# Kernel optimization log

Hardware: AMD Instinct MI355X
Metric: run time of the kernel (lower is better)

The kernel has to match this reference:

```python
import jax, jax.numpy as jnp
import numpy as np

B, T, D = 2, 2048, 1024
H = 16
DK = D // H


def setup_inputs() -> dict:
    key = jax.random.key(0)
    ks = jax.random.split(key, 5)
    s = 1.0 / np.sqrt(D)
    return {
        "x": jax.random.normal(ks[0], (B, T, D), dtype=jnp.float32),
        "Wq": jax.random.normal(ks[1], (D, D), dtype=jnp.float32) * s,
        "bq": jnp.zeros((D,), dtype=jnp.float32),
        "Wk": jax.random.normal(ks[2], (D, D), dtype=jnp.float32) * s,
        "bk": jnp.zeros((D,), dtype=jnp.float32),
        "Wv": jax.random.normal(ks[3], (D, D), dtype=jnp.float32) * s,
        "bv": jnp.zeros((D,), dtype=jnp.float32),
        "Wo": jax.random.normal(ks[4], (D, D), dtype=jnp.float32) * s,
        "bo": jnp.zeros((D,), dtype=jnp.float32),
    }


def reference(x, Wq, bq, Wk, bk, Wv, bv, Wo, bo):
    # projections (torch Linear: x @ W.T + b; here W is stored as (in, out))
    Q = x @ Wq + bq  # (B,T,D)
    K = x @ Wk + bk
    V = x @ Wv + bv
    # split heads -> (B,H,T,dk)
    Q = Q.reshape(B, T, H, DK).transpose(0, 2, 1, 3)
    K = K.reshape(B, T, H, DK).transpose(0, 2, 1, 3)
    V = V.reshape(B, T, H, DK).transpose(0, 2, 1, 3)
    scale = 1.0 / jnp.sqrt(jnp.asarray(DK, dtype=x.dtype))
    scores = jnp.einsum("bhqd,bhkd->bhqk", Q, K) * scale  # (B,H,T,T)
    causal = jnp.tril(jnp.ones((T, T), dtype=bool))
    scores = jnp.where(causal, scores, -jnp.inf)
    weights = jax.nn.softmax(scores, axis=-1)
    # dropout is identity in eval mode
    context = jnp.einsum("bhqk,bhkd->bhqd", weights, V)
    context = context.transpose(0, 2, 1, 3).reshape(B, T, D)
    return context @ Wo + bo
```

## Files before the change

kernel.cpp:

```cpp
#include <hip/hip_runtime.h>
#include <hip/hip_bf16.h>

constexpr int Bc = 2;
constexpr int Tc = 2048;
constexpr int Mc = Bc * Tc;

typedef __attribute__((ext_vector_type(8))) __bf16 bf16x8;
typedef __attribute__((ext_vector_type(4))) __bf16 bf16x4;
typedef __attribute__((ext_vector_type(4))) float floatx4;

__device__ __forceinline__ void gl_lds16(const void* g, void* l) {
    __builtin_amdgcn_global_load_lds(
        (const __attribute__((address_space(1))) void*)g,
        (__attribute__((address_space(3))) void*)l, 16, 0, 0);
}

__global__ __launch_bounds__(256) void prep_all(const float* __restrict__ x,
                                                const float* __restrict__ Wq,
                                                const float* __restrict__ Wk,
                                                const float* __restrict__ Wv,
                                                const float* __restrict__ Wo,
                                                __bf16* __restrict__ xb,
                                                __bf16* __restrict__ Wqkv,
                                                __bf16* __restrict__ Wot) {
    const int z = blockIdx.z;
    const int tid = threadIdx.x;
    if (z >= 4) {
        const int lb = blockIdx.y * 16 + blockIdx.x;
        const size_t base = ((size_t)(z - 4) * 256 + lb) * 4096;
#pragma unroll
        for (int it = 0; it < 4; ++it) {
            const size_t i = base + (size_t)(it * 256 + tid) * 4;
            const float4 v = *(const float4*)(x + i);
            bf16x4 r;
            r[0] = (__bf16)v.x; r[1] = (__bf16)v.y;
            r[2] = (__bf16)v.z; r[3] = (__bf16)v.w;
            *(bf16x4*)(xb + i) = r;
        }
        return;
    }
    __shared__ float t[64][65];
    const float* W = (z == 0) ? Wq : (z == 1) ? Wk : (z == 2) ? Wv : Wo;
    __bf16* Wt = (z < 3) ? Wqkv + (size_t)z * 1024 * 1024 : Wot;
    const int k0 = blockIdx.y * 64, n0 = blockIdx.x * 64;
    const int c = tid & 63, r0 = tid >> 6;
#pragma unroll
    for (int i = 0; i < 16; ++i)
        t[r0 + i * 4][c] = W[(size_t)(k0 + r0 + i * 4) * 1024 + n0 + c];
    __syncthreads();
#pragma unroll
    for (int i = 0; i < 16; ++i) {
        const int r = r0 + i * 4;
        Wt[(size_t)(n0 + r) * 1024 + k0 + c] = (__bf16)t[c][r];
    }
}

template <int TN, bool BF16_OUT, bool FUSE_VT>
__global__ __launch_bounds__(256) void gemm_bt(const __bf16* __restrict__ A,
                                               const __bf16* __restrict__ Bt,
                                               const float* __restrict__ b0,
                                               const float* __restrict__ b1,
                                               const float* __restrict__ b2,
                                               void* __restrict__ Cv,
                                               __bf16* __restrict__ Vt,
                                               int K, int ldc) {
    constexpr int NI = TN / 32;
    __shared__ __bf16 As[128 * 32];
    __shared__ __bf16 Bs[TN * 32];
    const int tid = threadIdx.x, lane = tid & 63, wave = tid >> 6;
    const int wm = wave & 1, wn = wave >> 1;
    const int bm = blockIdx.y * 128, bn = blockIdx.x * TN;
    const __bf16* Ab = A + (size_t)bm * K;
    const __bf16* Bb = Bt + (size_t)bn * K;
    const int quad = lane >> 4, tm = lane & 15;

    floatx4 acc[4][NI] = {};

    for (int k0 = 0; k0 < K; k0 += 32) {
#pragma unroll
        for (int i = 0; i < 2; ++i) {
            const int s = i * 256 + tid;
            gl_lds16(Ab + (size_t)(s >> 2) * K + k0 + (s & 3) * 8, As + s * 8);
        }
        if (TN == 128) {
#pragma unroll
            for (int i = 0; i < 2; ++i) {
                const int s = i * 256 + tid;
                gl_lds16(Bb + (size_t)(s >> 2) * K + k0 + (s & 3) * 8, Bs + s * 8);
            }
        } else {
            const int s = tid;
            gl_lds16(Bb + (size_t)(s >> 2) * K + k0 + (s & 3) * 8, Bs + s * 8);
        }
        __syncthreads();
        bf16x8 af[4], bfv[NI];
#pragma unroll
        for (int mi = 0; mi < 4; ++mi)
            af[mi] = *(const bf16x8*)(As + (wm * 64 + mi * 16 + tm) * 32 + quad * 8);
#pragma unroll
        for (int ni = 0; ni < NI; ++ni)
            bfv[ni] = *(const bf16x8*)(Bs + (wn * (TN / 2) + ni * 16 + tm) * 32 + quad * 8);
#pragma unroll
        for (int mi = 0; mi < 4; ++mi)
#pragma unroll
            for (int ni = 0; ni < NI; ++ni)
                acc[mi][ni] = __builtin_amdgcn_mfma_f32_16x16x32_bf16(
                    af[mi], bfv[ni], acc[mi][ni], 0, 0, 0);
        __syncthreads();
    }

#pragma unroll
    for (int ni = 0; ni < NI; ++ni) {
        const int gc = bn + wn * (TN / 2) + ni * 16 + tm;
        const float bias = (gc < 1024) ? b0[gc]
                         : (gc < 2048) ? b1[gc - 1024]
                                       : b2[gc - 2048];
#pragma unroll
        for (int mi = 0; mi < 4; ++mi) {
            const int gr0 = bm + wm * 64 + mi * 16 + quad * 4;
            if (FUSE_VT && gc >= 2048) {
                bf16x4 pv;
#pragma unroll
                for (int r = 0; r < 4; ++r) pv[r] = (__bf16)(acc[mi][ni][r] + bias);
                const int bb = gr0 >> 11, tloc = gr0 & 2047;
                const int hh = (gc - 2048) >> 6, dd = gc & 63;
                *(bf16x4*)(Vt + ((size_t)(bb * 16 + hh) * 64 + dd) * 2048 + tloc) = pv;
            } else if (BF16_OUT) {
#pragma unroll
                for (int r = 0; r < 4; ++r)
                    ((__bf16*)Cv)[(size_t)(gr0 + r) * ldc + gc] =
                        (__bf16)(acc[mi][ni][r] + bias);
            } else {
#pragma unroll
                for (int r = 0; r < 4; ++r)
                    ((float*)Cv)[(size_t)(gr0 + r) * ldc + gc] =
                        acc[mi][ni][r] + bias;
            }
        }
    }
}

__global__ __launch_bounds__(256) void attn_mfma(const __bf16* __restrict__ QK,
                                                 const __bf16* __restrict__ Vt,
                                                 __bf16* __restrict__ ctx) {
    constexpr float Cf = 0.18033688011112042f;
    constexpr float NEG = -1e30f;

    __shared__ __bf16 Ks[2][64 * 64];
    __shared__ __bf16 Vts[2][64 * 64];

    const int tid = threadIdx.x, lane = tid & 63, w = tid >> 6;
    const int c = lane & 15, quad = lane >> 4;
    const int bh = blockIdx.y, b = bh >> 4, h = bh & 15;
    const int flip = ((int)blockIdx.x & 1) ^ (((int)blockIdx.y >> 3) & 1);
    const int base = (((int)blockIdx.x >> 1) + ((int)blockIdx.y & 7)) & 15;
    const int qt = flip ? 31 - base : base;
    const int nk = qt + 1;

    const __bf16* Qb = QK + (size_t)(b * Tc) * 2048 + h * 64;
    const __bf16* Kb = Qb + 1024;
    const __bf16* Vtb = Vt + (size_t)bh * 64 * 2048;

    const __bf16* qr = Qb + (size_t)(qt * 64 + w * 16 + c) * 2048;
    const bf16x8 qf0 = *(const bf16x8*)(qr + quad * 8);
    const bf16x8 qf1 = *(const bf16x8*)(qr + 32 + quad * 8);

    float l = 0.f;
    floatx4 oa[4] = {};

    const int sw = c & 7;
    int koff0[4], koff1[4];
#pragma unroll
    for (int ni = 0; ni < 4; ++ni) {
        const int krow = ni * 16 + c;
        koff0[ni] = krow * 64 + (quad ^ sw) * 8;
        koff1[ni] = krow * 64 + ((4 + quad) ^ sw) * 8;
    }
    int voff0[4][2], voff1[4][2];
#pragma unroll
    for (int di = 0; di < 4; ++di) {
        const int vrow = di * 16 + c;
#pragma unroll
        for (int pr = 0; pr < 2; ++pr) {
            const int lc0 = (4 * pr + (quad >> 1)) ^ sw;
            const int lc1 = (4 * pr + 2 + (quad >> 1)) ^ sw;
            voff0[di][pr] = vrow * 64 + lc0 * 8 + (quad & 1) * 4;
            voff1[di][pr] = vrow * 64 + lc1 * 8 + (quad & 1) * 4;
        }
    }

    const int srow = tid >> 3;
    const int slc = (tid & 7) ^ (srow & 7);
    const __bf16* kg0 = Kb + (size_t)srow * 2048 + slc * 8;
    const __bf16* kg1 = kg0 + (size_t)32 * 2048;
    const __bf16* vg0 = Vtb + (size_t)srow * 2048 + slc * 8;
    const __bf16* vg1 = vg0 + (size_t)32 * 2048;

    gl_lds16(kg0, &Ks[0][tid * 8]);
    gl_lds16(kg1, &Ks[0][tid * 8 + 2048]);
    gl_lds16(vg0, &Vts[0][tid * 8]);
    gl_lds16(vg1, &Vts[0][tid * 8 + 2048]);
    kg0 += (size_t)64 * 2048; kg1 += (size_t)64 * 2048;
    vg0 += 64; vg1 += 64;
    __syncthreads();

    for (int kt = 0; kt < nk; ++kt) {
        const int buf = kt & 1;
        if (kt + 1 < nk) {
            __bf16* kd = &Ks[buf ^ 1][tid * 8];
            __bf16* vd = &Vts[buf ^ 1][tid * 8];
            gl_lds16(kg0, kd);
            gl_lds16(kg1, kd + 2048);
            gl_lds16(vg0, vd);
            gl_lds16(vg1, vd + 2048);
            kg0 += (size_t)64 * 2048; kg1 += (size_t)64 * 2048;
            vg0 += 64; vg1 += 64;
        }
        const __bf16* ks = Ks[buf];
        const __bf16* vs = Vts[buf];

        float sv[4][4];
#pragma unroll
        for (int ni = 0; ni < 4; ++ni) {
            const bf16x8 kb0 = *(const bf16x8*)(ks + koff0[ni]);
            const bf16x8 kb1 = *(const bf16x8*)(ks + koff1[ni]);
            floatx4 a = {};
            a = __builtin_amdgcn_mfma_f32_16x16x32_bf16(kb0, qf0, a, 0, 0, 0);
            a = __builtin_amdgcn_mfma_f32_16x16x32_bf16(kb1, qf1, a, 0, 0, 0);
#pragma unroll
            for (int r = 0; r < 4; ++r) sv[ni][r] = a[r];
        }

        if (kt == qt) {
#pragma unroll
            for (int ni = 0; ni < 4; ++ni)
#pragma unroll
                for (int r = 0; r < 4; ++r)
                    if (ni * 16 + quad * 4 + r > w * 16 + c) sv[ni][r] = NEG;
        }
        float sum = 0.f;
#pragma unroll
        for (int ni = 0; ni < 4; ++ni)
#pragma unroll
            for (int r = 0; r < 4; ++r) {
                const float p = __builtin_exp2f(sv[ni][r] * Cf);
                sv[ni][r] = p;
                sum += p;
            }
        sum += __shfl_xor(sum, 16);
        sum += __shfl_xor(sum, 32);
        l += sum;

        bf16x8 pb[2];
#pragma unroll
        for (int pr = 0; pr < 2; ++pr)
#pragma unroll
            for (int j = 0; j < 4; ++j) {
                pb[pr][j] = (__bf16)sv[pr * 2][j];
                pb[pr][4 + j] = (__bf16)sv[pr * 2 + 1][j];
            }

#pragma unroll
        for (int di = 0; di < 4; ++di) {
#pragma unroll
            for (int pr = 0; pr < 2; ++pr) {
                const bf16x4 va = *(const bf16x4*)(vs + voff0[di][pr]);
                const bf16x4 vb = *(const bf16x4*)(vs + voff1[di][pr]);
                bf16x8 vf;
#pragma unroll
                for (int j = 0; j < 4; ++j) { vf[j] = va[j]; vf[4 + j] = vb[j]; }
                oa[di] = __builtin_amdgcn_mfma_f32_16x16x32_bf16(
                    vf, pb[pr], oa[di], 0, 0, 0);
            }
        }
        __syncthreads();
    }

    const float inv = 1.f / l;
    __bf16* cp = ctx + (size_t)(b * Tc + qt * 64 + w * 16 + c) * 1024 +
                 h * 64 + quad * 4;
#pragma unroll
    for (int di = 0; di < 4; ++di) {
        bf16x4 rv;
#pragma unroll
        for (int r = 0; r < 4; ++r) rv[r] = (__bf16)(oa[di][r] * inv);
        *(bf16x4*)(cp + di * 16) = rv;
    }
}

extern "C" void kernel_launch(void* const* d_in, const int* in_sizes, int n_in,
                              void* d_out, int out_size, void* d_ws, size_t ws_size,
                              hipStream_t stream) {
    const float* x  = (const float*)d_in[0];
    const float* Wq = (const float*)d_in[1];
    const float* bq = (const float*)d_in[2];
    const float* Wk = (const float*)d_in[3];
    const float* bk = (const float*)d_in[4];
    const float* Wv = (const float*)d_in[5];
    const float* bv = (const float*)d_in[6];
    const float* Wo = (const float*)d_in[7];
    const float* bo = (const float*)d_in[8];

    __bf16* xb   = (__bf16*)d_ws;
    __bf16* Wqkv = xb + (size_t)Mc * 1024;
    __bf16* Wot  = Wqkv + (size_t)3072 * 1024;
    __bf16* QKb  = Wot + (size_t)1024 * 1024;
    __bf16* Vtw  = QKb + (size_t)Mc * 2048;
    __bf16* ctxb = xb;

    prep_all<<<dim3(16, 16, 8), 256, 0, stream>>>(x, Wq, Wk, Wv, Wo,
                                                  xb, Wqkv, Wot);

    gemm_bt<128, true, true><<<dim3(24, 32), 256, 0, stream>>>(
        xb, Wqkv, bq, bk, bv, QKb, Vtw, 1024, 2048);

    attn_mfma<<<dim3(32, 32), 256, 0, stream>>>(QKb, Vtw, ctxb);

    gemm_bt<64, false, false><<<dim3(16, 32), 256, 0, stream>>>(
        ctxb, Wot, bo, bo, bo, d_out, nullptr, 1024, 1024);
}
```

Baseline: 199.9 us.

## Deepen GEMM K-tile with swizzled LDS, prescale Q, permute Vt layout

The projection GEMM now stages a K-slice of 64 instead of 32 into LDS, with an XOR swizzle on columns to avoid bank conflicts, halving the number of barrier pairs per output tile. The softmax scale is folded into the Q projection epilogue, so attention skips a multiply per score. Vt is written in a permuted token order so attention can load each V fragment as a single 16-byte LDS read instead of two 8-byte reads plus a shuffle. The row-sum cross-lane reduction is deferred to the end of the loop. Larger LDS tiles may reduce occupancy, and rounding Q after scaling slightly changes numerics.

Result: faster. 189.2 us (-5.3%).

```diff
diff --git a/kernel.cpp b/kernel.cpp
--- a/kernel.cpp
+++ b/kernel.cpp
@@ -4,6 +4,7 @@
 constexpr int Bc = 2;
 constexpr int Tc = 2048;
 constexpr int Mc = Bc * Tc;
+constexpr float CfQ = 0.18033688011112042f;
 
 typedef __attribute__((ext_vector_type(8))) __bf16 bf16x8;
 typedef __attribute__((ext_vector_type(4))) __bf16 bf16x4;
@@ -65,47 +66,57 @@
                                                __bf16* __restrict__ Vt,
                                                int K, int ldc) {
     constexpr int NI = TN / 32;
-    __shared__ __bf16 As[128 * 32];
-    __shared__ __bf16 Bs[TN * 32];
+    __shared__ __bf16 As[128 * 64];
+    __shared__ __bf16 Bs[TN * 64];
     const int tid = threadIdx.x, lane = tid & 63, wave = tid >> 6;
     const int wm = wave & 1, wn = wave >> 1;
     const int bm = blockIdx.y * 128, bn = blockIdx.x * TN;
     const __bf16* Ab = A + (size_t)bm * K;
     const __bf16* Bb = Bt + (size_t)bn * K;
     const int quad = lane >> 4, tm = lane & 15;
+    const int tsw = tm & 7;
 
     floatx4 acc[4][NI] = {};
 
-    for (int k0 = 0; k0 < K; k0 += 32) {
-#pragma unroll
-        for (int i = 0; i < 2; ++i) {
+    for (int k0 = 0; k0 < K; k0 += 64) {
+#pragma unroll
+        for (int i = 0; i < 4; ++i) {
             const int s = i * 256 + tid;
-            gl_lds16(Ab + (size_t)(s >> 2) * K + k0 + (s & 3) * 8, As + s * 8);
-        }
-        if (TN == 128) {
-#pragma unroll
-            for (int i = 0; i < 2; ++i) {
-                const int s = i * 256 + tid;
-                gl_lds16(Bb + (size_t)(s >> 2) * K + k0 + (s & 3) * 8, Bs + s * 8);
-            }
-        } else {
-            const int s = tid;
-            gl_lds16(Bb + (size_t)(s >> 2) * K + k0 + (s & 3) * 8, Bs + s * 8);
+            const int row = s >> 3;
+            const int lc = (s & 7) ^ (row & 7);
+            gl_lds16(Ab + (size_t)row * K + k0 + lc * 8, As + s * 8);
+        }
+#pragma unroll
+        for (int i = 0; i < TN / 32; ++i) {
+            const int s = i * 256 + tid;
+            const int row = s >> 3;
+            const int lc = (s & 7) ^ (row & 7);
+            gl_lds16(Bb + (size_t)row * K + k0 + lc * 8, Bs + s * 8);
         }
         __syncthreads();
-        bf16x8 af[4], bfv[NI];
-#pragma unroll
-        for (int mi = 0; mi < 4; ++mi)
-            af[mi] = *(const bf16x8*)(As + (wm * 64 + mi * 16 + tm) * 32 + quad * 8);
-#pragma unroll
-        for (int ni = 0; ni < NI; ++ni)
-            bfv[ni] = *(const bf16x8*)(Bs + (wn * (TN / 2) + ni * 16 + tm) * 32 + quad * 8);
-#pragma unroll
-        for (int mi = 0; mi < 4; ++mi)
-#pragma unroll
-            for (int ni = 0; ni < NI; ++ni)
-                acc[mi][ni] = __builtin_amdgcn_mfma_f32_16x16x32_bf16(
-                    af[mi], bfv[ni], acc[mi][ni], 0, 0, 0);
+        bf16x8 af[4][2], bfv[NI][2];
+#pragma unroll
+        for (int mi = 0; mi < 4; ++mi) {
+            const int row = (wm * 64 + mi * 16 + tm) * 64;
+#pragma unroll
+            for (int ks = 0; ks < 2; ++ks)
+                af[mi][ks] = *(const bf16x8*)(As + row + ((ks * 4 + quad) ^ tsw) * 8);
+        }
+#pragma unroll
+        for (int ni = 0; ni < NI; ++ni) {
+            const int row = (wn * (TN / 2) + ni * 16 + tm) * 64;
+#pragma unroll
+            for (int ks = 0; ks < 2; ++ks)
+                bfv[ni][ks] = *(const bf16x8*)(Bs + row + ((ks * 4 + quad) ^ tsw) * 8);
+        }
+#pragma unroll
+        for (int ks = 0; ks < 2; ++ks)
+#pragma unroll
+            for (int mi = 0; mi < 4; ++mi)
+#pragma unroll
+                for (int ni = 0; ni < NI; ++ni)
+                    acc[mi][ni] = __builtin_amdgcn_mfma_f32_16x16x32_bf16(
+                        af[mi][ks], bfv[ni][ks], acc[mi][ni], 0, 0, 0);
         __syncthreads();
     }
 
@@ -115,6 +126,7 @@
         const float bias = (gc < 1024) ? b0[gc]
                          : (gc < 2048) ? b1[gc - 1024]
                                        : b2[gc - 2048];
+        const float scale = (FUSE_VT && gc < 1024) ? CfQ : 1.0f;
 #pragma unroll
         for (int mi = 0; mi < 4; ++mi) {
             const int gr0 = bm + wm * 64 + mi * 16 + quad * 4;
@@ -124,12 +136,14 @@
                 for (int r = 0; r < 4; ++r) pv[r] = (__bf16)(acc[mi][ni][r] + bias);
                 const int bb = gr0 >> 11, tloc = gr0 & 2047;
                 const int hh = (gc - 2048) >> 6, dd = gc & 63;
-                *(bf16x4*)(Vt + ((size_t)(bb * 16 + hh) * 64 + dd) * 2048 + tloc) = pv;
+                const int tperm = (tloc & ~63) + ((tloc >> 2) & 3) * 16 +
+                                  ((tloc >> 4) & 3) * 4;
+                *(bf16x4*)(Vt + ((size_t)(bb * 16 + hh) * 64 + dd) * 2048 + tperm) = pv;
             } else if (BF16_OUT) {
 #pragma unroll
                 for (int r = 0; r < 4; ++r)
                     ((__bf16*)Cv)[(size_t)(gr0 + r) * ldc + gc] =
-                        (__bf16)(acc[mi][ni][r] + bias);
+                        (__bf16)((acc[mi][ni][r] + bias) * scale);
             } else {
 #pragma unroll
                 for (int r = 0; r < 4; ++r)
@@ -143,7 +157,6 @@
 __global__ __launch_bounds__(256) void attn_mfma(const __bf16* __restrict__ QK,
                                                  const __bf16* __restrict__ Vt,
                                                  __bf16* __restrict__ ctx) {
-    constexpr float Cf = 0.18033688011112042f;
     constexpr float NEG = -1e30f;
 
     __shared__ __bf16 Ks[2][64 * 64];
@@ -165,7 +178,7 @@
     const bf16x8 qf0 = *(const bf16x8*)(qr + quad * 8);
     const bf16x8 qf1 = *(const bf16x8*)(qr + 32 + quad * 8);
 
-    float l = 0.f;
+    float lsum = 0.f;
     floatx4 oa[4] = {};
 
     const int sw = c & 7;
@@ -176,17 +189,13 @@
         koff0[ni] = krow * 64 + (quad ^ sw) * 8;
         koff1[ni] = krow * 64 + ((4 + quad) ^ sw) * 8;
     }
-    int voff0[4][2], voff1[4][2];
+    int voff[4][2];
 #pragma unroll
     for (int di = 0; di < 4; ++di) {
         const int vrow = di * 16 + c;
 #pragma unroll
-        for (int pr = 0; pr < 2; ++pr) {
-            const int lc0 = (4 * pr + (quad >> 1)) ^ sw;
-            const int lc1 = (4 * pr + 2 + (quad >> 1)) ^ sw;
-            voff0[di][pr] = vrow * 64 + lc0 * 8 + (quad & 1) * 4;
-            voff1[di][pr] = vrow * 64 + lc1 * 8 + (quad & 1) * 4;
-        }
+        for (int pr = 0; pr < 2; ++pr)
+            voff[di][pr] = vrow * 64 + ((quad * 2 + pr) ^ sw) * 8;
     }
 
     const int srow = tid >> 3;
@@ -238,18 +247,14 @@
                 for (int r = 0; r < 4; ++r)
                     if (ni * 16 + quad * 4 + r > w * 16 + c) sv[ni][r] = NEG;
         }
-        float sum = 0.f;
 #pragma unroll
         for (int ni = 0; ni < 4; ++ni)
 #pragma unroll
             for (int r = 0; r < 4; ++r) {
-                const float p = __builtin_exp2f(sv[ni][r] * Cf);
+                const float p = __builtin_exp2f(sv[ni][r]);
                 sv[ni][r] = p;
-                sum += p;
+                lsum += p;
             }
-        sum += __shfl_xor(sum, 16);
-        sum += __shfl_xor(sum, 32);
-        l += sum;
 
         bf16x8 pb[2];
 #pragma unroll
@@ -264,11 +269,7 @@
         for (int di = 0; di < 4; ++di) {
 #pragma unroll
             for (int pr = 0; pr < 2; ++pr) {
-                const bf16x4 va = *(const bf16x4*)(vs + voff0[di][pr]);
-                const bf16x4 vb = *(const bf16x4*)(vs + voff1[di][pr]);
-                bf16x8 vf;
-#pragma unroll
-                for (int j = 0; j < 4; ++j) { vf[j] = va[j]; vf[4 + j] = vb[j]; }
+                const bf16x8 vf = *(const bf16x8*)(vs + voff[di][pr]);
                 oa[di] = __builtin_amdgcn_mfma_f32_16x16x32_bf16(
                     vf, pb[pr], oa[di], 0, 0, 0);
             }
@@ -276,7 +277,9 @@
         __syncthreads();
     }
 
-    const float inv = 1.f / l;
+    lsum += __shfl_xor(lsum, 16);
+    lsum += __shfl_xor(lsum, 32);
+    const float inv = 1.f / lsum;
     __bf16* cp = ctx + (size_t)(b * Tc + qt * 64 + w * 16 + c) * 1024 +
                  h * 64 + quad * 4;
 #pragma unroll
```
